# Optimization experiments

Hardware: AMD Instinct MI355X
Metric: run time of the kernel (lower is better)

Reference implementation:

```python
import jax, jax.numpy as jnp
import numpy as np

SLOPE = 25.0  # fast_sigmoid surrogate slope
THR = 1.0     # snntorch Leaky default threshold

@jax.custom_vjp
def spike(x):
    # heaviside forward, fast-sigmoid surrogate backward
    return (x > 0).astype(x.dtype)

def _spike_fwd(x):
    return spike(x), x

def _spike_bwd(x, g):
    return (g / (SLOPE * jnp.abs(x) + 1.0) ** 2,)

spike.defvjp(_spike_fwd, _spike_bwd)


def _xavier(k, shape):
    fan_out, fan_in = shape
    lim = np.sqrt(6.0 / (fan_in + fan_out)).astype(np.float32)
    return jax.random.uniform(k, shape, jnp.float32, -lim, lim)


def setup_inputs() -> dict:
    key = jax.random.key(0)
    ks = jax.random.split(key, 6)
    B, T, NI, H1, H2, NO = 256, 100, 512, 1024, 1024, 10
    return {
        "x": jax.random.normal(ks[0], (B, T, NI), jnp.float32),
        "W1": _xavier(ks[1], (H1, NI)),
        "W1r": _xavier(ks[2], (H1, H1)),
        "W2": _xavier(ks[3], (H2, H1)),
        "W2r": _xavier(ks[4], (H2, H2)),
        "Wout": _xavier(ks[5], (NO, H2)),
        "beta1": jnp.float32(0.9),
        "beta2": jnp.float32(0.9),
        "beta_out": jnp.float32(0.9),
    }


def reference(x, W1, W1r, W2, W2r, Wout, beta1, beta2, beta_out):
    B, T, NI = x.shape
    H1, H2, NO = W1.shape[0], W2.shape[0], Wout.shape[0]
    b1 = jnp.clip(beta1, 0.0, 1.0)
    b2 = jnp.clip(beta2, 0.0, 1.0)
    bo = jnp.clip(beta_out, 0.0, 1.0)
    xt = jnp.transpose(x, (1, 0, 2))  # [T, B, NI]

    def step(carry, x_t):
        mem1, spk1, mem2, spk2, mem_out = carry
        # layer 1: feedforward + recurrent current, leaky integrate, subtract-reset
        cur1 = x_t @ W1.T + spk1 @ W1r.T
        reset1 = jax.lax.stop_gradient((mem1 > THR).astype(mem1.dtype))
        mem1 = b1 * mem1 + cur1 - reset1 * THR
        spk1 = spike(mem1 - THR)
        # layer 2
        cur2 = spk1 @ W2.T + spk2 @ W2r.T
        reset2 = jax.lax.stop_gradient((mem2 > THR).astype(mem2.dtype))
        mem2 = b2 * mem2 + cur2 - reset2 * THR
        spk2 = spike(mem2 - THR)
        # readout: reset_mechanism='none'
        mem_out = bo * mem_out + spk2 @ Wout.T
        return (mem1, spk1, mem2, spk2, mem_out), (spk1, mem_out)

    z = lambda n: jnp.zeros((B, n), x.dtype)
    carry0 = (z(H1), z(H1), z(H2), z(H2), z(NO))
    _, (spk1_rec, mem_out_rec) = jax.lax.scan(step, carry0, xt)
    return spk1_rec, mem_out_rec  # [T,B,H1], [T,B,NO]
```

## Files before the change

### kernel.cpp

```cpp
#include <hip/hip_runtime.h>

#define S_ELE (256 * 1024)
#define NBLK 512
#define GRP  8
#define GSZ  (NBLK / GRP)

typedef float f32x4 __attribute__((ext_vector_type(4)));

struct Ptrs {
    const float *x, *W1, *W1r, *W2, *W2r, *Wout;
    const float *b1, *b2, *bo;
    float *spk1_rec, *mout_rec;
    float *mem1, *mem2, *memo;
    float *w1rt, *w2t, *w2rt, *xw, *S2;
    unsigned *bar, *cnt1, *cnt2;
    unsigned short *idx1, *idx2;
    int t_ch;
};

__device__ __forceinline__ float clip01(float b) { return fminf(fmaxf(b, 0.0f), 1.0f); }
__device__ __forceinline__ float4 ld4(const float* p) { return *reinterpret_cast<const float4*>(p); }
__device__ __forceinline__ void   st4(float* p, float4 v) { *reinterpret_cast<float4*>(p) = v; }
__device__ __forceinline__ void   st4nt(float* p, float4 v)
{
    f32x4 n = { v.x, v.y, v.z, v.w };
    __builtin_nontemporal_store(n, reinterpret_cast<f32x4*>(p));
}

__device__ __forceinline__ float4 memup(float4 mo, float4 cur, float b, float4* sv)
{
    float4 mn, s;
    mn.x = b * mo.x + cur.x - (mo.x > 1.0f ? 1.0f : 0.0f); s.x = (mn.x - 1.0f) > 0.0f ? 1.0f : 0.0f;
    mn.y = b * mo.y + cur.y - (mo.y > 1.0f ? 1.0f : 0.0f); s.y = (mn.y - 1.0f) > 0.0f ? 1.0f : 0.0f;
    mn.z = b * mo.z + cur.z - (mo.z > 1.0f ? 1.0f : 0.0f); s.z = (mn.z - 1.0f) > 0.0f ? 1.0f : 0.0f;
    mn.w = b * mo.w + cur.w - (mo.w > 1.0f ? 1.0f : 0.0f); s.w = (mn.w - 1.0f) > 0.0f ? 1.0f : 0.0f;
    *sv = s; return mn;
}

__device__ __forceinline__ void gbar(unsigned* bar)
{
    __syncthreads();
    if (threadIdx.x == 0) {
        unsigned g = __hip_atomic_load(&bar[0], __ATOMIC_RELAXED, __HIP_MEMORY_SCOPE_AGENT);
        unsigned* gc = &bar[8 + ((int)blockIdx.x & (GRP - 1)) * 32];
        unsigned a = __hip_atomic_fetch_add(gc, 1u, __ATOMIC_ACQ_REL, __HIP_MEMORY_SCOPE_AGENT);
        if (a == GSZ - 1) {
            __hip_atomic_store(gc, 0u, __ATOMIC_RELAXED, __HIP_MEMORY_SCOPE_AGENT);
            unsigned tp = __hip_atomic_fetch_add(&bar[1], 1u, __ATOMIC_ACQ_REL, __HIP_MEMORY_SCOPE_AGENT);
            if (tp == GRP - 1) {
                __hip_atomic_store(&bar[1], 0u, __ATOMIC_RELAXED, __HIP_MEMORY_SCOPE_AGENT);
                __hip_atomic_store(&bar[0], g + 1u, __ATOMIC_RELEASE, __HIP_MEMORY_SCOPE_AGENT);
            }
        }
        while (__hip_atomic_load(&bar[0], __ATOMIC_ACQUIRE, __HIP_MEMORY_SCOPE_AGENT) == g)
            __builtin_amdgcn_s_sleep(2);
    }
    __syncthreads();
}

__device__ __forceinline__ void tr32(float* sm, const float* src, float* dst, int tr, int tc)
{
    const int t = (int)threadIdx.x;
    const int r = t >> 3, c4 = (t & 7) << 2;
    __syncthreads();
    float4 v = ld4(src + (size_t)(tr * 32 + r) * 1024 + tc * 32 + c4);
    sm[r * 33 + c4 + 0] = v.x; sm[r * 33 + c4 + 1] = v.y;
    sm[r * 33 + c4 + 2] = v.z; sm[r * 33 + c4 + 3] = v.w;
    __syncthreads();
    const int kk = t >> 3, nn4 = (t & 7) << 2;
    float4 o;
    o.x = sm[(nn4 + 0) * 33 + kk]; o.y = sm[(nn4 + 1) * 33 + kk];
    o.z = sm[(nn4 + 2) * 33 + kk]; o.w = sm[(nn4 + 3) * 33 + kk];
    st4(dst + (size_t)(tc * 32 + kk) * 1024 + tr * 32 + nn4, o);
}

__device__ __forceinline__ void xw_tile(float* sm, const float* xA, const float* W1,
                                        float* out, int tm, int tn)
{
    float* As = sm;
    float* Bs = sm + 1056;
    const int t = (int)threadIdx.x;
    const int ar = t >> 1;
    const int ak = (t & 1) << 2;
    const int r0 = (t >> 4) << 3;
    const int c0 = (t & 15) << 3;
    const float* Ab = xA + (size_t)(tm * 128) * 51200;
    const float* Bb = W1 + (size_t)(tn * 128) * 512;
    float4 pa = ld4(Ab + (size_t)ar * 51200 + ak);
    float4 pb = ld4(Bb + (size_t)ar * 512 + ak);
    float acc[8][8] = {};
    for (int c = 0; c < 64; ++c) {
        __syncthreads();
        As[(ak + 0) * 132 + ar] = pa.x; As[(ak + 1) * 132 + ar] = pa.y;
        As[(ak + 2) * 132 + ar] = pa.z; As[(ak + 3) * 132 + ar] = pa.w;
        Bs[(ak + 0) * 132 + ar] = pb.x; Bs[(ak + 1) * 132 + ar] = pb.y;
        Bs[(ak + 2) * 132 + ar] = pb.z; Bs[(ak + 3) * 132 + ar] = pb.w;
        __syncthreads();
        if (c + 1 < 64) {
            const int ko = (c + 1) * 8;
            pa = ld4(Ab + (size_t)ar * 51200 + ko + ak);
            pb = ld4(Bb + (size_t)ar * 512 + ko + ak);
        }
        #pragma unroll
        for (int k = 0; k < 8; ++k) {
            float4 a0 = ld4(&As[k * 132 + r0]);
            float4 a1 = ld4(&As[k * 132 + r0 + 4]);
            float4 b0 = ld4(&Bs[k * 132 + c0]);
            float4 b1 = ld4(&Bs[k * 132 + c0 + 4]);
            float av[8] = {a0.x, a0.y, a0.z, a0.w, a1.x, a1.y, a1.z, a1.w};
            float bv[8] = {b0.x, b0.y, b0.z, b0.w, b1.x, b1.y, b1.z, b1.w};
            #pragma unroll
            for (int i = 0; i < 8; ++i)
                #pragma unroll
                for (int j = 0; j < 8; ++j)
                    acc[i][j] = fmaf(av[i], bv[j], acc[i][j]);
        }
    }
    #pragma unroll
    for (int i = 0; i < 8; ++i) {
        float* row = out + (size_t)(tm * 128 + r0 + i) * 1024 + tn * 128 + c0;
        st4(row,     make_float4(acc[i][0], acc[i][1], acc[i][2], acc[i][3]));
        st4(row + 4, make_float4(acc[i][4], acc[i][5], acc[i][6], acc[i][7]));
    }
}

template <int NC>
__device__ __forceinline__ void gatherN(const unsigned short* const lp[],
    const unsigned st[], const unsigned en[], const float* Wt, int n4, float4 c[])
{
    unsigned j[NC], e[NC];
    float4 pa[NC], pb[NC];
    #pragma unroll
    for (int q = 0; q < NC; ++q) {
        j[q] = st[q]; e[q] = en[q];
        c[q] = make_float4(0.f, 0.f, 0.f, 0.f);
        if (j[q] < e[q])     pa[q] = ld4(Wt + (size_t)lp[q][j[q]] * 1024 + n4);
        if (j[q] + 1 < e[q]) pb[q] = ld4(Wt + (size_t)lp[q][j[q] + 1] * 1024 + n4);
    }
    for (;;) {
        bool any = false;
        #pragma unroll
        for (int q = 0; q < NC; ++q) {
            if (j[q] < e[q]) {
                float4 v = pa[q];
                pa[q] = pb[q];
                if (j[q] + 2 < e[q]) pb[q] = ld4(Wt + (size_t)lp[q][j[q] + 2] * 1024 + n4);
                c[q].x += v.x; c[q].y += v.y; c[q].z += v.z; c[q].w += v.w;
                ++j[q];
                any = any || (j[q] < e[q]);
            }
        }
        if (!any) break;
    }
}

__device__ __forceinline__ void build_list(const float* s_spk,
    unsigned short* gidx, unsigned* gcnt)
{
    const int l = (int)threadIdx.x;
    unsigned tot = 0, prev = 0;
    #pragma unroll
    for (int i = 0; i < 16; ++i) {
        float s = s_spk[i * 64 + l];
        unsigned long long m = __ballot(s != 0.0f);
        unsigned off = (unsigned)__popcll(m & ((1ull << l) - 1ull));
        if (s != 0.0f) gidx[tot + off] = (unsigned short)(i * 64 + l);
        tot += (unsigned)__popcll(m);
        if (i & 1) { if (l == 0) gcnt[i >> 1] = tot - prev; prev = tot; }
    }
}

__device__ __forceinline__ void l1_full(float* sm, const Ptrs& p, int r, int tau)
{
    const int t = (int)threadIdx.x, n4 = t << 2;
    const int pp = 1 - (tau & 1);
    const unsigned* cw = p.cnt1 + ((size_t)pp * 256 + r) * 8;
    unsigned pos[9];
    pos[0] = 0;
    #pragma unroll
    for (int w = 0; w < 8; ++w) pos[w + 1] = pos[w] + cw[w];
    unsigned* sl = (unsigned*)(sm + 1024);
    const unsigned* gl = (const unsigned*)(p.idx1 + ((size_t)pp * 256 + r) * 1024);
    for (unsigned i = t; i < ((pos[8] + 1) >> 1); i += 256) sl[i] = gl[i];
    __syncthreads();
    const unsigned short* sl16 = (const unsigned short*)sl;
    const unsigned short* lp[8];
    unsigned st[8], en[8];
    #pragma unroll
    for (int q = 0; q < 8; ++q) { lp[q] = sl16; st[q] = pos[q]; en[q] = pos[q + 1]; }
    float4 c[8];
    gatherN<8>(lp, st, en, p.w1rt, n4, c);

    const size_t base = (size_t)r * 1024 + n4;
    const int slot = tau % p.t_ch;
    float4 acc = ld4(p.xw + (size_t)slot * S_ELE + base);
    #pragma unroll
    for (int w = 0; w < 8; ++w) {
        acc.x += c[w].x; acc.y += c[w].y; acc.z += c[w].z; acc.w += c[w].w;
    }
    const float bb = clip01(*p.b1);
    float4 mo = ld4(p.mem1 + base);
    float4 sv; float4 mn = memup(mo, acc, bb, &sv);
    st4(p.mem1 + base, mn);
    st4nt(p.spk1_rec + (size_t)tau * S_ELE + base, sv);
    sm[n4 + 0] = sv.x; sm[n4 + 1] = sv.y; sm[n4 + 2] = sv.z; sm[n4 + 3] = sv.w;
    __syncthreads();
    if (t < 64) build_list(sm, p.idx1 + ((size_t)(tau & 1) * 256 + r) * 1024,
                           p.cnt1 + ((size_t)(tau & 1) * 256 + r) * 8);
}

__device__ __forceinline__ void l2g4(float* sm, const Ptrs& p, int g, int fam, int step)
{
    const int t = (int)threadIdx.x, n4 = t << 2;
    const bool rsel = fam >= 2;
    const bool hi = fam & 1;
    const int par = rsel ? (1 - (step & 1)) : (step & 1);
    const unsigned* cbase = (rsel ? p.cnt2 : p.cnt1) + (size_t)par * 256 * 8;
    const unsigned short* ibase = (rsel ? p.idx2 : p.idx1) + (size_t)par * 256 * 1024;
    const float* W = rsel ? p.w2rt : p.w2t;

    const unsigned short* lp[4];
    unsigned st[4], en[4];
    #pragma unroll
    for (int q = 0; q < 4; ++q) {
        const int r = 4 * g + q;
        const unsigned* cw = cbase + (size_t)r * 8;
        unsigned nlo = cw[0] + cw[1] + cw[2] + cw[3];
        unsigned tot = nlo + cw[4] + cw[5] + cw[6] + cw[7];
        unsigned* sl = (unsigned*)sm + 512 * q;
        const unsigned* gl = (const unsigned*)(ibase + (size_t)r * 1024);
        for (unsigned i = t; i < ((tot + 1) >> 1); i += 256) sl[i] = gl[i];
        lp[q] = (const unsigned short*)sl;
        st[q] = hi ? nlo : 0;
        en[q] = hi ? tot : nlo;
    }
    __syncthreads();
    float4 c[4];
    gatherN<4>(lp, st, en, W, n4, c);
    #pragma unroll
    for (int q = 0; q < 4; ++q)
        st4(p.S2 + (size_t)fam * S_ELE + (size_t)(4 * g + q) * 1024 + n4, c[q]);
}

__device__ __forceinline__ void upd2_row(float* sm, const Ptrs& p, int r, int step)
{
    const int t = (int)threadIdx.x, n4 = t << 2;
    const size_t base = (size_t)r * 1024 + n4;
    float4 p0 = ld4(p.S2 + base);
    float4 p1 = ld4(p.S2 + (size_t)S_ELE + base);
    float4 p2 = ld4(p.S2 + (size_t)2 * S_ELE + base);
    float4 p3 = ld4(p.S2 + (size_t)3 * S_ELE + base);
    float4 cur;
    cur.x = (p0.x + p1.x) + (p2.x + p3.x);
    cur.y = (p0.y + p1.y) + (p2.y + p3.y);
    cur.z = (p0.z + p1.z) + (p2.z + p3.z);
    cur.w = (p0.w + p1.w) + (p2.w + p3.w);
    const float bb = clip01(*p.b2);
    float4 mo = ld4(p.mem2 + base);
    float4 sv; float4 mn = memup(mo, cur, bb, &sv);
    st4(p.mem2 + base, mn);
    sm[n4 + 0] = sv.x; sm[n4 + 1] = sv.y; sm[n4 + 2] = sv.z; sm[n4 + 3] = sv.w;
    __syncthreads();
    if (t < 64) build_list(sm, p.idx2 + ((size_t)(step & 1) * 256 + r) * 1024,
                           p.cnt2 + ((size_t)(step & 1) * 256 + r) * 8);
    const int wave = t >> 6, lane = t & 63;
    const float bo = clip01(*p.bo);
    float v[16];
    #pragma unroll
    for (int i = 0; i < 16; ++i) v[i] = sm[lane + 64 * i];
    float* rec = p.mout_rec + (size_t)step * 2560;
    for (int o = wave; o < 10; o += 4) {
        float sum = 0.0f;
        #pragma unroll
        for (int i = 0; i < 16; ++i)
            sum = fmaf(v[i], p.Wout[o * 1024 + lane + 64 * i], sum);
        #pragma unroll
        for (int off = 32; off > 0; off >>= 1) sum += __shfl_down(sum, off);
        if (lane == 0) {
            const float m = bo * p.memo[r * 10 + o] + sum;
            p.memo[r * 10 + o] = m;
            __builtin_nontemporal_store(m, &rec[r * 10 + o]);
        }
    }
}

__global__ __launch_bounds__(256, 2) void snn_all(Ptrs p)
{
    __shared__ float sm[2176];
    const int bid = (int)blockIdx.x;
    const int x = bid & 7, g = bid >> 3;

    for (int task = bid; task < 3072; task += NBLK) {
        const float* src = task < 1024 ? p.W1r : (task < 2048 ? p.W2 : p.W2r);
        float* dst = task < 1024 ? p.w1rt : (task < 2048 ? p.w2t : p.w2rt);
        const int id = task & 1023;
        tr32(sm, src, dst, id >> 5, id & 31);
    }
    gbar(p.bar);

    for (int tau = 0; tau <= 100; ++tau) {
        if (tau < 100 && (tau % p.t_ch) == 0) {
            const int ntask = p.t_ch * 16;
            for (int task = bid; task < ntask; task += NBLK) {
                const int tp = task >> 4, tile = task & 15;
                xw_tile(sm, p.x + (size_t)(tau + tp) * 512, p.W1,
                        p.xw + (size_t)tp * S_ELE, tile >> 3, tile & 7);
            }
            gbar(p.bar);
        }
        if (x < 4) { if (tau < 100) l1_full(sm, p, g * 4 + x, tau); }
        else       { if (tau >= 1)  l2g4(sm, p, g, x - 4, tau - 1); }
        gbar(p.bar);
        if (x >= 4 && tau >= 1) upd2_row(sm, p, g * 4 + (x - 4), tau - 1);
        gbar(p.bar);
    }
}

__global__ __launch_bounds__(256, 2) void fb_pre(Ptrs p)
{
    __shared__ float sm[2176];
    for (int task = blockIdx.x; task < 3072; task += gridDim.x) {
        const float* src = task < 1024 ? p.W1r : (task < 2048 ? p.W2 : p.W2r);
        float* dst = task < 1024 ? p.w1rt : (task < 2048 ? p.w2t : p.w2rt);
        const int id = task & 1023;
        tr32(sm, src, dst, id >> 5, id & 31);
    }
}

__global__ __launch_bounds__(256, 2) void fb_xw(Ptrs p, int t0)
{
    __shared__ float sm[2176];
    const int task = (int)blockIdx.x;
    const int tp = task >> 4, tile = task & 15;
    xw_tile(sm, p.x + (size_t)(t0 + tp) * 512, p.W1,
            p.xw + (size_t)tp * S_ELE, tile >> 3, tile & 7);
}

__global__ __launch_bounds__(256, 2) void fb_p1(Ptrs p, int tau)
{
    __shared__ float sm[2176];
    const int bid = (int)blockIdx.x;
    const int x = bid & 7, g = bid >> 3;
    if (x < 4) { if (tau < 100) l1_full(sm, p, g * 4 + x, tau); }
    else       { if (tau >= 1)  l2g4(sm, p, g, x - 4, tau - 1); }
}

__global__ __launch_bounds__(256, 2) void fb_p2(Ptrs p, int tau)
{
    __shared__ float sm[2176];
    if (tau >= 1) upd2_row(sm, p, (int)blockIdx.x, tau - 1);
}

extern "C" void kernel_launch(void* const* d_in, const int* in_sizes, int n_in,
                              void* d_out, int out_size, void* d_ws, size_t ws_size,
                              hipStream_t stream)
{
    Ptrs p;
    p.x    = (const float*)d_in[0];
    p.W1   = (const float*)d_in[1];
    p.W1r  = (const float*)d_in[2];
    p.W2   = (const float*)d_in[3];
    p.W2r  = (const float*)d_in[4];
    p.Wout = (const float*)d_in[5];
    p.b1   = (const float*)d_in[6];
    p.b2   = (const float*)d_in[7];
    p.bo   = (const float*)d_in[8];

    float* out = (float*)d_out;
    p.spk1_rec = out;
    p.mout_rec = out + (size_t)100 * S_ELE;

    float* w = (float*)d_ws;
    p.mem1 = w;  w += S_ELE;
    p.mem2 = w;  w += S_ELE;
    p.memo = w;  w += 2560;
    p.bar  = (unsigned*)w;  w += 512;
    p.cnt1 = (unsigned*)w;  w += 4096;
    p.cnt2 = (unsigned*)w;  w += 4096;
    p.idx1 = (unsigned short*)w;  w += 262144;
    p.idx2 = (unsigned short*)w;  w += 262144;
    p.w1rt = w;  w += 1048576;
    p.w2t  = w;  w += 1048576;
    p.w2rt = w;  w += 1048576;
    p.S2   = w;  w += 4 * S_ELE;
    p.xw   = w;

    const size_t used = (size_t)(w - (float*)d_ws) * sizeof(float);
    int t_ch = 1;
    const int cands[] = {100, 50, 25, 20, 10, 5, 4, 2, 1};
    for (int c : cands)
        if (used + (size_t)c * S_ELE * sizeof(float) <= ws_size) { t_ch = c; break; }
    p.t_ch = t_ch;

    (void)hipMemsetAsync(p.mem1, 0,
                   ((size_t)2 * S_ELE + 2560 + 512 + 8192) * sizeof(float), stream);

    int maxb = 0;
    hipError_t qerr = hipOccupancyMaxActiveBlocksPerMultiprocessor(
        &maxb, (const void*)snn_all, 256, 0);
    bool coop = (qerr == hipSuccess && maxb >= 2);

    if (coop) {
        void* args[] = { (void*)&p };
        if (hipLaunchCooperativeKernel((const void*)snn_all, dim3(NBLK), dim3(256),
                                       args, 0, stream) != hipSuccess)
            coop = false;
    }

    if (!coop) {
        hipLaunchKernelGGL(fb_pre, dim3(NBLK), dim3(256), 0, stream, p);
        for (int tau = 0; tau <= 100; ++tau) {
            if (tau < 100 && (tau % t_ch) == 0)
                hipLaunchKernelGGL(fb_xw, dim3(t_ch * 16), dim3(256), 0, stream, p, tau);
            hipLaunchKernelGGL(fb_p1, dim3(NBLK), dim3(256), 0, stream, p, tau);
            hipLaunchKernelGGL(fb_p2, dim3(256), dim3(256), 0, stream, p, tau);
        }
    }
}
```

Before: 4.299 ms.

## Double persistent grid and split layer-1 rows into column halves

Raises the cooperative grid from 512 to 1024 blocks with four blocks per CU, so each layer-1 row is handled by two blocks covering half the columns with float2 gathers. Layer-2 partial gathers now cover two rows per block instead of four. Spike index lists change to fixed 128-entry segments per 128-neuron window, so half-row blocks can write their segments independently. The aim is more parallelism and latency hiding in the sparse recurrent gathers, at the cost of more blocks in each grid barrier, tighter register limits, and duplicated index staging.

```diff
diff --git a/kernel.cpp b/kernel.cpp
--- a/kernel.cpp
+++ b/kernel.cpp
@@ -1,11 +1,12 @@
 #include <hip/hip_runtime.h>
 
 #define S_ELE (256 * 1024)
-#define NBLK 512
+#define NBLK 1024
 #define GRP  8
 #define GSZ  (NBLK / GRP)
 
 typedef float f32x4 __attribute__((ext_vector_type(4)));
+typedef float f32x2 __attribute__((ext_vector_type(2)));
 
 struct Ptrs {
     const float *x, *W1, *W1r, *W2, *W2r, *Wout;
@@ -21,10 +22,12 @@
 __device__ __forceinline__ float clip01(float b) { return fminf(fmaxf(b, 0.0f), 1.0f); }
 __device__ __forceinline__ float4 ld4(const float* p) { return *reinterpret_cast<const float4*>(p); }
 __device__ __forceinline__ void   st4(float* p, float4 v) { *reinterpret_cast<float4*>(p) = v; }
-__device__ __forceinline__ void   st4nt(float* p, float4 v)
-{
-    f32x4 n = { v.x, v.y, v.z, v.w };
-    __builtin_nontemporal_store(n, reinterpret_cast<f32x4*>(p));
+__device__ __forceinline__ float2 ld2(const float* p) { return *reinterpret_cast<const float2*>(p); }
+__device__ __forceinline__ void   st2(float* p, float2 v) { *reinterpret_cast<float2*>(p) = v; }
+__device__ __forceinline__ void   st2nt(float* p, float2 v)
+{
+    f32x2 n = { v.x, v.y };
+    __builtin_nontemporal_store(n, reinterpret_cast<f32x2*>(p));
 }
 
 __device__ __forceinline__ float4 memup(float4 mo, float4 cur, float b, float4* sv)
@@ -34,6 +37,13 @@
     mn.y = b * mo.y + cur.y - (mo.y > 1.0f ? 1.0f : 0.0f); s.y = (mn.y - 1.0f) > 0.0f ? 1.0f : 0.0f;
     mn.z = b * mo.z + cur.z - (mo.z > 1.0f ? 1.0f : 0.0f); s.z = (mn.z - 1.0f) > 0.0f ? 1.0f : 0.0f;
     mn.w = b * mo.w + cur.w - (mo.w > 1.0f ? 1.0f : 0.0f); s.w = (mn.w - 1.0f) > 0.0f ? 1.0f : 0.0f;
+    *sv = s; return mn;
+}
+__device__ __forceinline__ float2 memup2(float2 mo, float2 cur, float b, float2* sv)
+{
+    float2 mn, s;
+    mn.x = b * mo.x + cur.x - (mo.x > 1.0f ? 1.0f : 0.0f); s.x = (mn.x - 1.0f) > 0.0f ? 1.0f : 0.0f;
+    mn.y = b * mo.y + cur.y - (mo.y > 1.0f ? 1.0f : 0.0f); s.y = (mn.y - 1.0f) > 0.0f ? 1.0f : 0.0f;
     *sv = s; return mn;
 }
 
@@ -154,62 +164,122 @@
     }
 }
 
-__device__ __forceinline__ void build_list(const float* s_spk,
+__device__ __forceinline__ void gather8_2(const unsigned short* lst,
+    const unsigned pos[9], const float* Wt, int col, float2 c[8])
+{
+    unsigned j[8], e[8];
+    float2 pa[8], pb[8];
+    #pragma unroll
+    for (int q = 0; q < 8; ++q) {
+        j[q] = pos[q]; e[q] = pos[q + 1];
+        c[q] = make_float2(0.f, 0.f);
+        if (j[q] < e[q])     pa[q] = ld2(Wt + (size_t)lst[j[q]] * 1024 + col);
+        if (j[q] + 1 < e[q]) pb[q] = ld2(Wt + (size_t)lst[j[q] + 1] * 1024 + col);
+    }
+    for (;;) {
+        bool any = false;
+        #pragma unroll
+        for (int q = 0; q < 8; ++q) {
+            if (j[q] < e[q]) {
+                float2 v = pa[q];
+                pa[q] = pb[q];
+                if (j[q] + 2 < e[q]) pb[q] = ld2(Wt + (size_t)lst[j[q] + 2] * 1024 + col);
+                c[q].x += v.x; c[q].y += v.y;
+                ++j[q];
+                any = any || (j[q] < e[q]);
+            }
+        }
+        if (!any) break;
+    }
+}
+
+__device__ __forceinline__ void build_seg_full(const float* s_spk,
     unsigned short* gidx, unsigned* gcnt)
 {
     const int l = (int)threadIdx.x;
-    unsigned tot = 0, prev = 0;
-    #pragma unroll
-    for (int i = 0; i < 16; ++i) {
-        float s = s_spk[i * 64 + l];
-        unsigned long long m = __ballot(s != 0.0f);
-        unsigned off = (unsigned)__popcll(m & ((1ull << l) - 1ull));
-        if (s != 0.0f) gidx[tot + off] = (unsigned short)(i * 64 + l);
-        tot += (unsigned)__popcll(m);
-        if (i & 1) { if (l == 0) gcnt[i >> 1] = tot - prev; prev = tot; }
-    }
-}
-
-__device__ __forceinline__ void l1_full(float* sm, const Ptrs& p, int r, int tau)
-{
-    const int t = (int)threadIdx.x, n4 = t << 2;
+    #pragma unroll
+    for (int w = 0; w < 8; ++w) {
+        unsigned wtot = 0;
+        #pragma unroll
+        for (int i = 0; i < 2; ++i) {
+            const int grp = w * 2 + i;
+            float s = s_spk[grp * 64 + l];
+            unsigned long long m = __ballot(s != 0.0f);
+            unsigned off = (unsigned)__popcll(m & ((1ull << l) - 1ull));
+            if (s != 0.0f) gidx[w * 128 + wtot + off] = (unsigned short)(grp * 64 + l);
+            wtot += (unsigned)__popcll(m);
+        }
+        if (l == 0) gcnt[w] = wtot;
+    }
+}
+
+__device__ __forceinline__ void build_seg_half(const float* s_half, int h,
+    unsigned short* gidx, unsigned* gcnt)
+{
+    const int l = (int)threadIdx.x;
+    #pragma unroll
+    for (int wl = 0; wl < 4; ++wl) {
+        const int w = 4 * h + wl;
+        unsigned wtot = 0;
+        #pragma unroll
+        for (int i = 0; i < 2; ++i) {
+            const int grp = wl * 2 + i;
+            float s = s_half[grp * 64 + l];
+            unsigned long long m = __ballot(s != 0.0f);
+            unsigned off = (unsigned)__popcll(m & ((1ull << l) - 1ull));
+            if (s != 0.0f)
+                gidx[w * 128 + wtot + off] = (unsigned short)(h * 512 + grp * 64 + l);
+            wtot += (unsigned)__popcll(m);
+        }
+        if (l == 0) gcnt[w] = wtot;
+    }
+}
+
+__device__ __forceinline__ void stage_list(unsigned short* sl,
+    const unsigned short* gseg, const unsigned* cw, const unsigned pos[9])
+{
+    const int t = (int)threadIdx.x;
+    #pragma unroll
+    for (int w = 0; w < 8; ++w)
+        for (unsigned i = t; i < cw[w]; i += 256)
+            sl[pos[w] + i] = gseg[w * 128 + i];
+}
+
+__device__ __forceinline__ void l1_half(float* sm, const Ptrs& p, int r, int h, int tau)
+{
+    const int t = (int)threadIdx.x;
+    const int lc = t * 2;
+    const int col = h * 512 + lc;
     const int pp = 1 - (tau & 1);
     const unsigned* cw = p.cnt1 + ((size_t)pp * 256 + r) * 8;
     unsigned pos[9];
     pos[0] = 0;
     #pragma unroll
     for (int w = 0; w < 8; ++w) pos[w + 1] = pos[w] + cw[w];
-    unsigned* sl = (unsigned*)(sm + 1024);
-    const unsigned* gl = (const unsigned*)(p.idx1 + ((size_t)pp * 256 + r) * 1024);
-    for (unsigned i = t; i < ((pos[8] + 1) >> 1); i += 256) sl[i] = gl[i];
-    __syncthreads();
-    const unsigned short* sl16 = (const unsigned short*)sl;
-    const unsigned short* lp[8];
-    unsigned st[8], en[8];
-    #pragma unroll
-    for (int q = 0; q < 8; ++q) { lp[q] = sl16; st[q] = pos[q]; en[q] = pos[q + 1]; }
-    float4 c[8];
-    gatherN<8>(lp, st, en, p.w1rt, n4, c);
-
-    const size_t base = (size_t)r * 1024 + n4;
+    unsigned short* sl16 = (unsigned short*)(sm + 512);
+    stage_list(sl16, p.idx1 + ((size_t)pp * 256 + r) * 1024, cw, pos);
+    __syncthreads();
+
+    float2 c[8];
+    gather8_2(sl16, pos, p.w1rt, col, c);
+
+    const size_t base = (size_t)r * 1024 + col;
     const int slot = tau % p.t_ch;
-    float4 acc = ld4(p.xw + (size_t)slot * S_ELE + base);
-    #pragma unroll
-    for (int w = 0; w < 8; ++w) {
-        acc.x += c[w].x; acc.y += c[w].y; acc.z += c[w].z; acc.w += c[w].w;
-    }
+    float2 acc = ld2(p.xw + (size_t)slot * S_ELE + base);
+    #pragma unroll
+    for (int w = 0; w < 8; ++w) { acc.x += c[w].x; acc.y += c[w].y; }
     const float bb = clip01(*p.b1);
-    float4 mo = ld4(p.mem1 + base);
-    float4 sv; float4 mn = memup(mo, acc, bb, &sv);
-    st4(p.mem1 + base, mn);
-    st4nt(p.spk1_rec + (size_t)tau * S_ELE + base, sv);
-    sm[n4 + 0] = sv.x; sm[n4 + 1] = sv.y; sm[n4 + 2] = sv.z; sm[n4 + 3] = sv.w;
-    __syncthreads();
-    if (t < 64) build_list(sm, p.idx1 + ((size_t)(tau & 1) * 256 + r) * 1024,
-                           p.cnt1 + ((size_t)(tau & 1) * 256 + r) * 8);
-}
-
-__device__ __forceinline__ void l2g4(float* sm, const Ptrs& p, int g, int fam, int step)
+    float2 mo = ld2(p.mem1 + base);
+    float2 sv; float2 mn = memup2(mo, acc, bb, &sv);
+    st2(p.mem1 + base, mn);
+    st2nt(p.spk1_rec + (size_t)tau * S_ELE + base, sv);
+    sm[lc] = sv.x; sm[lc + 1] = sv.y;
+    __syncthreads();
+    if (t < 64) build_seg_half(sm, h, p.idx1 + ((size_t)(tau & 1) * 256 + r) * 1024,
+                               p.cnt1 + ((size_t)(tau & 1) * 256 + r) * 8);
+}
+
+__device__ __forceinline__ void l2g2(float* sm, const Ptrs& p, int g, int fam, int step)
 {
     const int t = (int)threadIdx.x, n4 = t << 2;
     const bool rsel = fam >= 2;
@@ -219,27 +289,28 @@
     const unsigned short* ibase = (rsel ? p.idx2 : p.idx1) + (size_t)par * 256 * 1024;
     const float* W = rsel ? p.w2rt : p.w2t;
 
-    const unsigned short* lp[4];
-    unsigned st[4], en[4];
-    #pragma unroll
-    for (int q = 0; q < 4; ++q) {
-        const int r = 4 * g + q;
+    const unsigned short* lp[2];
+    unsigned st[2], en[2];
+    #pragma unroll
+    for (int q = 0; q < 2; ++q) {
+        const int r = 2 * g + q;
         const unsigned* cw = cbase + (size_t)r * 8;
-        unsigned nlo = cw[0] + cw[1] + cw[2] + cw[3];
-        unsigned tot = nlo + cw[4] + cw[5] + cw[6] + cw[7];
-        unsigned* sl = (unsigned*)sm + 512 * q;
-        const unsigned* gl = (const unsigned*)(ibase + (size_t)r * 1024);
-        for (unsigned i = t; i < ((tot + 1) >> 1); i += 256) sl[i] = gl[i];
-        lp[q] = (const unsigned short*)sl;
-        st[q] = hi ? nlo : 0;
-        en[q] = hi ? tot : nlo;
-    }
-    __syncthreads();
-    float4 c[4];
-    gatherN<4>(lp, st, en, W, n4, c);
-    #pragma unroll
-    for (int q = 0; q < 4; ++q)
-        st4(p.S2 + (size_t)fam * S_ELE + (size_t)(4 * g + q) * 1024 + n4, c[q]);
+        unsigned pos[9];
+        pos[0] = 0;
+        #pragma unroll
+        for (int w = 0; w < 8; ++w) pos[w + 1] = pos[w] + cw[w];
+        unsigned short* sl = (unsigned short*)sm + 1024 * q;
+        stage_list(sl, ibase + (size_t)r * 1024, cw, pos);
+        lp[q] = sl;
+        st[q] = hi ? pos[4] : 0;
+        en[q] = hi ? pos[8] : pos[4];
+    }
+    __syncthreads();
+    float4 c[2];
+    gatherN<2>(lp, st, en, W, n4, c);
+    #pragma unroll
+    for (int q = 0; q < 2; ++q)
+        st4(p.S2 + (size_t)fam * S_ELE + (size_t)(2 * g + q) * 1024 + n4, c[q]);
 }
 
 __device__ __forceinline__ void upd2_row(float* sm, const Ptrs& p, int r, int step)
@@ -261,8 +332,8 @@
     st4(p.mem2 + base, mn);
     sm[n4 + 0] = sv.x; sm[n4 + 1] = sv.y; sm[n4 + 2] = sv.z; sm[n4 + 3] = sv.w;
     __syncthreads();
-    if (t < 64) build_list(sm, p.idx2 + ((size_t)(step & 1) * 256 + r) * 1024,
-                           p.cnt2 + ((size_t)(step & 1) * 256 + r) * 8);
+    if (t < 64) build_seg_full(sm, p.idx2 + ((size_t)(step & 1) * 256 + r) * 1024,
+                               p.cnt2 + ((size_t)(step & 1) * 256 + r) * 8);
     const int wave = t >> 6, lane = t & 63;
     const float bo = clip01(*p.bo);
     float v[16];
@@ -284,7 +355,7 @@
     }
 }
 
-__global__ __launch_bounds__(256, 2) void snn_all(Ptrs p)
+__global__ __launch_bounds__(256, 4) void snn_all(Ptrs p)
 {
     __shared__ float sm[2176];
     const int bid = (int)blockIdx.x;
@@ -308,15 +379,21 @@
             }
             gbar(p.bar);
         }
-        if (x < 4) { if (tau < 100) l1_full(sm, p, g * 4 + x, tau); }
-        else       { if (tau >= 1)  l2g4(sm, p, g, x - 4, tau - 1); }
+        if (x < 4) {
+            if (tau < 100) {
+                const int idx = x * 128 + g;
+                l1_half(sm, p, idx >> 1, idx & 1, tau);
+            }
+        } else {
+            if (tau >= 1) l2g2(sm, p, g, x - 4, tau - 1);
+        }
         gbar(p.bar);
-        if (x >= 4 && tau >= 1) upd2_row(sm, p, g * 4 + (x - 4), tau - 1);
+        if (bid < 256 && tau >= 1) upd2_row(sm, p, bid, tau - 1);
         gbar(p.bar);
     }
 }
 
-__global__ __launch_bounds__(256, 2) void fb_pre(Ptrs p)
+__global__ __launch_bounds__(256, 4) void fb_pre(Ptrs p)
 {
     __shared__ float sm[2176];
     for (int task = blockIdx.x; task < 3072; task += gridDim.x) {
@@ -327,7 +404,7 @@
     }
 }
 
-__global__ __launch_bounds__(256, 2) void fb_xw(Ptrs p, int t0)
+__global__ __launch_bounds__(256, 4) void fb_xw(Ptrs p, int t0)
 {
     __shared__ float sm[2176];
     const int task = (int)blockIdx.x;
@@ -336,16 +413,22 @@
             p.xw + (size_t)tp * S_ELE, tile >> 3, tile & 7);
 }
 
-__global__ __launch_bounds__(256, 2) void fb_p1(Ptrs p, int tau)
+__global__ __launch_bounds__(256, 4) void fb_p1(Ptrs p, int tau)
 {
     __shared__ float sm[2176];
     const int bid = (int)blockIdx.x;
     const int x = bid & 7, g = bid >> 3;
-    if (x < 4) { if (tau < 100) l1_full(sm, p, g * 4 + x, tau); }
-    else       { if (tau >= 1)  l2g4(sm, p, g, x - 4, tau - 1); }
-}
-
-__global__ __launch_bounds__(256, 2) void fb_p2(Ptrs p, int tau)
+    if (x < 4) {
+        if (tau < 100) {
+            const int idx = x * 128 + g;
+            l1_half(sm, p, idx >> 1, idx & 1, tau);
+        }
+    } else {
+        if (tau >= 1) l2g2(sm, p, g, x - 4, tau - 1);
+    }
+}
+
+__global__ __launch_bounds__(256, 4) void fb_p2(Ptrs p, int tau)
 {
     __shared__ float sm[2176];
     if (tau >= 1) upd2_row(sm, p, (int)blockIdx.x, tau - 1);
@@ -398,7 +481,7 @@
     int maxb = 0;
     hipError_t qerr = hipOccupancyMaxActiveBlocksPerMultiprocessor(
         &maxb, (const void*)snn_all, 256, 0);
-    bool coop = (qerr == hipSuccess && maxb >= 2);
+    bool coop = (qerr == hipSuccess && maxb >= 4);
 
     if (coop) {
         void* args[] = { (void*)&p };
```

Result: faster. 4.024 ms (-6.4%).

## Replace sparse spike-gather recurrences with dense split-K FMA over transposed spikes

Applied to the files above, without the earlier changes.

Replaces the ballot-built spike index lists and sparse row gathers with dense matrix-vector style FMA loops. Each block computes a K-half partial against spikes stored transposed (sT1/sT2), and the partial planes are reduced in a separate update phase. The change doubles the cooperative grid to 1024 blocks at 4 blocks per CU, and half of those blocks idle in phase 1. The spike matrices become dense, which removes the data-dependent gather imbalance. In exchange it does far more arithmetic and weight traffic and adds eight extra partial-sum planes of memory.

```diff
diff --git a/kernel.cpp b/kernel.cpp
--- a/kernel.cpp
+++ b/kernel.cpp
@@ -1,7 +1,7 @@
 #include <hip/hip_runtime.h>
 
 #define S_ELE (256 * 1024)
-#define NBLK 512
+#define NBLK 1024
 #define GRP  8
 #define GSZ  (NBLK / GRP)
 
@@ -12,9 +12,8 @@
     const float *b1, *b2, *bo;
     float *spk1_rec, *mout_rec;
     float *mem1, *mem2, *memo;
-    float *w1rt, *w2t, *w2rt, *xw, *S2;
-    unsigned *bar, *cnt1, *cnt2;
-    unsigned short *idx1, *idx2;
+    float *w1rt, *w2t, *w2rt, *xw, *P1, *S2, *sT1, *sT2;
+    unsigned *bar;
     int t_ch;
 };
 
@@ -124,122 +123,97 @@
     }
 }
 
-template <int NC>
-__device__ __forceinline__ void gatherN(const unsigned short* const lp[],
-    const unsigned st[], const unsigned en[], const float* Wt, int n4, float4 c[])
-{
-    unsigned j[NC], e[NC];
-    float4 pa[NC], pb[NC];
+__device__ __forceinline__ void l1_dense(const Ptrs& p, int cs, int j, int tau)
+{
+    const int t   = (int)threadIdx.x;
+    const int g0  = (j & 31) * 8;
+    const int kh  = j >> 5;
+    const int col = cs * 256 + t;
+    const int k0  = kh * 512;
+
+    const float* wp = p.w1rt + (size_t)k0 * 1024 + col;
+    const float* sp = p.sT1  + (size_t)k0 * 256 + g0;
+
+    #pragma unroll 1
+    for (int w = 0; w < 4; ++w) {
+        float c[8] = {};
+        #pragma unroll 4
+        for (int kk = 0; kk < 128; ++kk) {
+            const float wv = *wp;
+            float4 sa = ld4(sp);
+            float4 sb = ld4(sp + 4);
+            c[0] = fmaf(wv, sa.x, c[0]); c[1] = fmaf(wv, sa.y, c[1]);
+            c[2] = fmaf(wv, sa.z, c[2]); c[3] = fmaf(wv, sa.w, c[3]);
+            c[4] = fmaf(wv, sb.x, c[4]); c[5] = fmaf(wv, sb.y, c[5]);
+            c[6] = fmaf(wv, sb.z, c[6]); c[7] = fmaf(wv, sb.w, c[7]);
+            wp += 1024; sp += 256;
+        }
+        const int wi = kh * 4 + w;
+        float* P = p.P1 + (size_t)wi * S_ELE + (size_t)g0 * 1024 + col;
+        #pragma unroll
+        for (int g = 0; g < 8; ++g) P[(size_t)g * 1024] = c[g];
+    }
+}
+
+__device__ __forceinline__ void l2_dense(const Ptrs& p, int xp, int j, int rsel)
+{
+    const int t     = (int)threadIdx.x;
+    const int group = j >> 2;
+    const int kh    = (j >> 1) & 1;
+    const int cs    = (xp << 1) | (j & 1);
+    const int g0    = group * 16;
+    const int col   = cs * 256 + t;
+    const int k0    = kh * 512;
+
+    const float* W  = rsel ? p.w2rt : p.w2t;
+    const float* sT = rsel ? p.sT2  : p.sT1;
+    const float* wp = W  + (size_t)k0 * 1024 + col;
+    const float* sp = sT + (size_t)k0 * 256 + g0;
+
+    float c[16] = {};
+    #pragma unroll 2
+    for (int kk = 0; kk < 512; ++kk) {
+        const float wv = *wp;
+        float4 s0 = ld4(sp);
+        float4 s1 = ld4(sp + 4);
+        float4 s2 = ld4(sp + 8);
+        float4 s3 = ld4(sp + 12);
+        c[0]  = fmaf(wv, s0.x, c[0]);  c[1]  = fmaf(wv, s0.y, c[1]);
+        c[2]  = fmaf(wv, s0.z, c[2]);  c[3]  = fmaf(wv, s0.w, c[3]);
+        c[4]  = fmaf(wv, s1.x, c[4]);  c[5]  = fmaf(wv, s1.y, c[5]);
+        c[6]  = fmaf(wv, s1.z, c[6]);  c[7]  = fmaf(wv, s1.w, c[7]);
+        c[8]  = fmaf(wv, s2.x, c[8]);  c[9]  = fmaf(wv, s2.y, c[9]);
+        c[10] = fmaf(wv, s2.z, c[10]); c[11] = fmaf(wv, s2.w, c[11]);
+        c[12] = fmaf(wv, s3.x, c[12]); c[13] = fmaf(wv, s3.y, c[13]);
+        c[14] = fmaf(wv, s3.z, c[14]); c[15] = fmaf(wv, s3.w, c[15]);
+        wp += 1024; sp += 256;
+    }
+    const int plane = rsel * 2 + kh;
+    float* S = p.S2 + (size_t)plane * S_ELE + (size_t)g0 * 1024 + col;
     #pragma unroll
-    for (int q = 0; q < NC; ++q) {
-        j[q] = st[q]; e[q] = en[q];
-        c[q] = make_float4(0.f, 0.f, 0.f, 0.f);
-        if (j[q] < e[q])     pa[q] = ld4(Wt + (size_t)lp[q][j[q]] * 1024 + n4);
-        if (j[q] + 1 < e[q]) pb[q] = ld4(Wt + (size_t)lp[q][j[q] + 1] * 1024 + n4);
-    }
-    for (;;) {
-        bool any = false;
-        #pragma unroll
-        for (int q = 0; q < NC; ++q) {
-            if (j[q] < e[q]) {
-                float4 v = pa[q];
-                pa[q] = pb[q];
-                if (j[q] + 2 < e[q]) pb[q] = ld4(Wt + (size_t)lp[q][j[q] + 2] * 1024 + n4);
-                c[q].x += v.x; c[q].y += v.y; c[q].z += v.z; c[q].w += v.w;
-                ++j[q];
-                any = any || (j[q] < e[q]);
-            }
-        }
-        if (!any) break;
-    }
-}
-
-__device__ __forceinline__ void build_list(const float* s_spk,
-    unsigned short* gidx, unsigned* gcnt)
-{
-    const int l = (int)threadIdx.x;
-    unsigned tot = 0, prev = 0;
-    #pragma unroll
-    for (int i = 0; i < 16; ++i) {
-        float s = s_spk[i * 64 + l];
-        unsigned long long m = __ballot(s != 0.0f);
-        unsigned off = (unsigned)__popcll(m & ((1ull << l) - 1ull));
-        if (s != 0.0f) gidx[tot + off] = (unsigned short)(i * 64 + l);
-        tot += (unsigned)__popcll(m);
-        if (i & 1) { if (l == 0) gcnt[i >> 1] = tot - prev; prev = tot; }
-    }
-}
-
-__device__ __forceinline__ void l1_full(float* sm, const Ptrs& p, int r, int tau)
+    for (int g = 0; g < 16; ++g) S[(size_t)g * 1024] = c[g];
+}
+
+__device__ __forceinline__ void upd1_row(const Ptrs& p, int r, int tau)
 {
     const int t = (int)threadIdx.x, n4 = t << 2;
-    const int pp = 1 - (tau & 1);
-    const unsigned* cw = p.cnt1 + ((size_t)pp * 256 + r) * 8;
-    unsigned pos[9];
-    pos[0] = 0;
-    #pragma unroll
-    for (int w = 0; w < 8; ++w) pos[w + 1] = pos[w] + cw[w];
-    unsigned* sl = (unsigned*)(sm + 1024);
-    const unsigned* gl = (const unsigned*)(p.idx1 + ((size_t)pp * 256 + r) * 1024);
-    for (unsigned i = t; i < ((pos[8] + 1) >> 1); i += 256) sl[i] = gl[i];
-    __syncthreads();
-    const unsigned short* sl16 = (const unsigned short*)sl;
-    const unsigned short* lp[8];
-    unsigned st[8], en[8];
-    #pragma unroll
-    for (int q = 0; q < 8; ++q) { lp[q] = sl16; st[q] = pos[q]; en[q] = pos[q + 1]; }
-    float4 c[8];
-    gatherN<8>(lp, st, en, p.w1rt, n4, c);
-
     const size_t base = (size_t)r * 1024 + n4;
     const int slot = tau % p.t_ch;
     float4 acc = ld4(p.xw + (size_t)slot * S_ELE + base);
     #pragma unroll
     for (int w = 0; w < 8; ++w) {
-        acc.x += c[w].x; acc.y += c[w].y; acc.z += c[w].z; acc.w += c[w].w;
+        float4 q = ld4(p.P1 + (size_t)w * S_ELE + base);
+        acc.x += q.x; acc.y += q.y; acc.z += q.z; acc.w += q.w;
     }
     const float bb = clip01(*p.b1);
     float4 mo = ld4(p.mem1 + base);
     float4 sv; float4 mn = memup(mo, acc, bb, &sv);
     st4(p.mem1 + base, mn);
     st4nt(p.spk1_rec + (size_t)tau * S_ELE + base, sv);
-    sm[n4 + 0] = sv.x; sm[n4 + 1] = sv.y; sm[n4 + 2] = sv.z; sm[n4 + 3] = sv.w;
-    __syncthreads();
-    if (t < 64) build_list(sm, p.idx1 + ((size_t)(tau & 1) * 256 + r) * 1024,
-                           p.cnt1 + ((size_t)(tau & 1) * 256 + r) * 8);
-}
-
-__device__ __forceinline__ void l2g4(float* sm, const Ptrs& p, int g, int fam, int step)
-{
-    const int t = (int)threadIdx.x, n4 = t << 2;
-    const bool rsel = fam >= 2;
-    const bool hi = fam & 1;
-    const int par = rsel ? (1 - (step & 1)) : (step & 1);
-    const unsigned* cbase = (rsel ? p.cnt2 : p.cnt1) + (size_t)par * 256 * 8;
-    const unsigned short* ibase = (rsel ? p.idx2 : p.idx1) + (size_t)par * 256 * 1024;
-    const float* W = rsel ? p.w2rt : p.w2t;
-
-    const unsigned short* lp[4];
-    unsigned st[4], en[4];
-    #pragma unroll
-    for (int q = 0; q < 4; ++q) {
-        const int r = 4 * g + q;
-        const unsigned* cw = cbase + (size_t)r * 8;
-        unsigned nlo = cw[0] + cw[1] + cw[2] + cw[3];
-        unsigned tot = nlo + cw[4] + cw[5] + cw[6] + cw[7];
-        unsigned* sl = (unsigned*)sm + 512 * q;
-        const unsigned* gl = (const unsigned*)(ibase + (size_t)r * 1024);
-        for (unsigned i = t; i < ((tot + 1) >> 1); i += 256) sl[i] = gl[i];
-        lp[q] = (const unsigned short*)sl;
-        st[q] = hi ? nlo : 0;
-        en[q] = hi ? tot : nlo;
-    }
-    __syncthreads();
-    float4 c[4];
-    gatherN<4>(lp, st, en, W, n4, c);
-    #pragma unroll
-    for (int q = 0; q < 4; ++q)
-        st4(p.S2 + (size_t)fam * S_ELE + (size_t)(4 * g + q) * 1024 + n4, c[q]);
+    p.sT1[(size_t)(n4 + 0) * 256 + r] = sv.x;
+    p.sT1[(size_t)(n4 + 1) * 256 + r] = sv.y;
+    p.sT1[(size_t)(n4 + 2) * 256 + r] = sv.z;
+    p.sT1[(size_t)(n4 + 3) * 256 + r] = sv.w;
 }
 
 __device__ __forceinline__ void upd2_row(float* sm, const Ptrs& p, int r, int step)
@@ -259,10 +233,12 @@
     float4 mo = ld4(p.mem2 + base);
     float4 sv; float4 mn = memup(mo, cur, bb, &sv);
     st4(p.mem2 + base, mn);
+    p.sT2[(size_t)(n4 + 0) * 256 + r] = sv.x;
+    p.sT2[(size_t)(n4 + 1) * 256 + r] = sv.y;
+    p.sT2[(size_t)(n4 + 2) * 256 + r] = sv.z;
+    p.sT2[(size_t)(n4 + 3) * 256 + r] = sv.w;
     sm[n4 + 0] = sv.x; sm[n4 + 1] = sv.y; sm[n4 + 2] = sv.z; sm[n4 + 3] = sv.w;
     __syncthreads();
-    if (t < 64) build_list(sm, p.idx2 + ((size_t)(step & 1) * 256 + r) * 1024,
-                           p.cnt2 + ((size_t)(step & 1) * 256 + r) * 8);
     const int wave = t >> 6, lane = t & 63;
     const float bo = clip01(*p.bo);
     float v[16];
@@ -284,11 +260,20 @@
     }
 }
 
-__global__ __launch_bounds__(256, 2) void snn_all(Ptrs p)
+__device__ __forceinline__ void phase1(const Ptrs& p, int bid, int tau)
+{
+    const int x = bid & 7, g = bid >> 3;
+    if (g & 1) return;
+    const int j = g >> 1;
+    if (x < 4)      { if (tau < 100) l1_dense(p, x, j, tau); }
+    else if (x < 6) { if (tau >= 1)  l2_dense(p, x - 4, j, 0); }
+    else            { if (tau >= 1)  l2_dense(p, x - 6, j, 1); }
+}
+
+__global__ __launch_bounds__(256, 4) void snn_all(Ptrs p)
 {
     __shared__ float sm[2176];
     const int bid = (int)blockIdx.x;
-    const int x = bid & 7, g = bid >> 3;
 
     for (int task = bid; task < 3072; task += NBLK) {
         const float* src = task < 1024 ? p.W1r : (task < 2048 ? p.W2 : p.W2r);
@@ -308,15 +293,15 @@
             }
             gbar(p.bar);
         }
-        if (x < 4) { if (tau < 100) l1_full(sm, p, g * 4 + x, tau); }
-        else       { if (tau >= 1)  l2g4(sm, p, g, x - 4, tau - 1); }
+        phase1(p, bid, tau);
         gbar(p.bar);
-        if (x >= 4 && tau >= 1) upd2_row(sm, p, g * 4 + (x - 4), tau - 1);
+        if (bid < 256)      { if (tau < 100) upd1_row(p, bid, tau); }
+        else if (bid < 512) { if (tau >= 1)  upd2_row(sm, p, bid - 256, tau - 1); }
         gbar(p.bar);
     }
 }
 
-__global__ __launch_bounds__(256, 2) void fb_pre(Ptrs p)
+__global__ __launch_bounds__(256, 4) void fb_pre(Ptrs p)
 {
     __shared__ float sm[2176];
     for (int task = blockIdx.x; task < 3072; task += gridDim.x) {
@@ -327,7 +312,7 @@
     }
 }
 
-__global__ __launch_bounds__(256, 2) void fb_xw(Ptrs p, int t0)
+__global__ __launch_bounds__(256, 4) void fb_xw(Ptrs p, int t0)
 {
     __shared__ float sm[2176];
     const int task = (int)blockIdx.x;
@@ -336,19 +321,17 @@
             p.xw + (size_t)tp * S_ELE, tile >> 3, tile & 7);
 }
 
-__global__ __launch_bounds__(256, 2) void fb_p1(Ptrs p, int tau)
+__global__ __launch_bounds__(256, 4) void fb_p1(Ptrs p, int tau)
+{
+    phase1(p, (int)blockIdx.x, tau);
+}
+
+__global__ __launch_bounds__(256, 4) void fb_p2(Ptrs p, int tau)
 {
     __shared__ float sm[2176];
     const int bid = (int)blockIdx.x;
-    const int x = bid & 7, g = bid >> 3;
-    if (x < 4) { if (tau < 100) l1_full(sm, p, g * 4 + x, tau); }
-    else       { if (tau >= 1)  l2g4(sm, p, g, x - 4, tau - 1); }
-}
-
-__global__ __launch_bounds__(256, 2) void fb_p2(Ptrs p, int tau)
-{
-    __shared__ float sm[2176];
-    if (tau >= 1) upd2_row(sm, p, (int)blockIdx.x, tau - 1);
+    if (bid < 256)      { if (tau < 100) upd1_row(p, bid, tau); }
+    else if (bid < 512) { if (tau >= 1)  upd2_row(sm, p, bid - 256, tau - 1); }
 }
 
 extern "C" void kernel_launch(void* const* d_in, const int* in_sizes, int n_in,
@@ -375,13 +358,12 @@
     p.mem2 = w;  w += S_ELE;
     p.memo = w;  w += 2560;
     p.bar  = (unsigned*)w;  w += 512;
-    p.cnt1 = (unsigned*)w;  w += 4096;
-    p.cnt2 = (unsigned*)w;  w += 4096;
-    p.idx1 = (unsigned short*)w;  w += 262144;
-    p.idx2 = (unsigned short*)w;  w += 262144;
+    p.sT1  = w;  w += 262144;
+    p.sT2  = w;  w += 262144;
     p.w1rt = w;  w += 1048576;
     p.w2t  = w;  w += 1048576;
     p.w2rt = w;  w += 1048576;
+    p.P1   = w;  w += 8 * S_ELE;
     p.S2   = w;  w += 4 * S_ELE;
     p.xw   = w;
 
@@ -393,12 +375,12 @@
     p.t_ch = t_ch;
 
     (void)hipMemsetAsync(p.mem1, 0,
-                   ((size_t)2 * S_ELE + 2560 + 512 + 8192) * sizeof(float), stream);
+        ((size_t)2 * S_ELE + 2560 + 512 + 2 * 262144) * sizeof(float), stream);
 
     int maxb = 0;
     hipError_t qerr = hipOccupancyMaxActiveBlocksPerMultiprocessor(
         &maxb, (const void*)snn_all, 256, 0);
-    bool coop = (qerr == hipSuccess && maxb >= 2);
+    bool coop = (qerr == hipSuccess && maxb >= 4);
 
     if (coop) {
         void* args[] = { (void*)&p };
@@ -413,7 +395,7 @@
             if (tau < 100 && (tau % t_ch) == 0)
                 hipLaunchKernelGGL(fb_xw, dim3(t_ch * 16), dim3(256), 0, stream, p, tau);
             hipLaunchKernelGGL(fb_p1, dim3(NBLK), dim3(256), 0, stream, p, tau);
-            hipLaunchKernelGGL(fb_p2, dim3(256), dim3(256), 0, stream, p, tau);
-        }
-    }
-}
+            hipLaunchKernelGGL(fb_p2, dim3(512), dim3(256), 0, stream, p, tau);
+        }
+    }
+}
```

Measured after the change: 14.94 ms. 248% more time.
